# Performance work log

Hardware: AMD Instinct MI355X
Metric: run time of the kernel (lower is better)

The kernel has to match this reference:

```python
import jax, jax.numpy as jnp
import numpy as np

B, L, E, H = 1, 2048, 512, 8
D = E // H


def setup_inputs() -> dict:
    key = jax.random.key(0)
    k0, k1, k2 = jax.random.split(key, 3)
    x = jax.random.normal(k0, (B, L, E), jnp.float32)
    W_qkv = jax.random.normal(k1, (E, 3 * E), jnp.float32) / np.sqrt(E).astype(np.float32)
    b_qkv = jnp.zeros((3 * E,), jnp.float32)
    W_out = jax.random.normal(k2, (E, E), jnp.float32) / np.sqrt(E).astype(np.float32)
    b_out = jnp.zeros((E,), jnp.float32)
    return {"x": x, "W_qkv": W_qkv, "b_qkv": b_qkv, "W_out": W_out, "b_out": b_out}


def reference(x, W_qkv, b_qkv, W_out, b_out):
    num_heads = H
    eps = 1e-6
    b, l, e = x.shape
    d = e // num_heads
    qkv = x @ W_qkv + b_qkv                      # [B, L, 3E]
    q, k, v = jnp.split(qkv, 3, axis=-1)
    q = q.reshape(b, l, num_heads, d).transpose(0, 2, 1, 3)  # [B,H,L,D]
    k = k.reshape(b, l, num_heads, d).transpose(0, 2, 1, 3)
    v = v.reshape(b, l, num_heads, d).transpose(0, 2, 1, 3)
    pos = jnp.arange(l, dtype=jnp.float32).reshape(1, 1, l, 1)
    cos_w = jnp.cos(jnp.pi / 2 * pos / l)
    sin_w = jnp.sin(jnp.pi / 2 * pos / l)
    q_prime = jax.nn.relu(q)
    k_prime = jax.nn.relu(k)

    def branch(w):
        qw = q_prime * w                          # [B,H,L,D]
        kw = k_prime * w
        kv = jnp.einsum('bhld,bhle->bhlde', kw, v)  # causal running KV state
        kv_cum = jnp.cumsum(kv, axis=2)
        ctx = jnp.einsum('bhld,bhlde->bhle', qw, kv_cum)
        nrm = jnp.einsum('bhld,bhld->bhl', qw, jnp.cumsum(kw, axis=2))
        return ctx, nrm

    ctx_cos, nrm_cos = branch(cos_w)
    ctx_sin, nrm_sin = branch(sin_w)
    out = (ctx_cos + ctx_sin) / ((nrm_cos + nrm_sin)[..., None] + eps)
    out = out.transpose(0, 2, 1, 3).reshape(b, l, e)
    return out @ W_out + b_out
```

## Files before the change

kernel.cpp:

```cpp
#include <hip/hip_runtime.h>

constexpr int L_SEQ = 2048;
constexpr int E_DIM = 512;
constexpr int H_NUM = 8;
constexpr int QKV_W = 3 * E_DIM;
constexpr int CHK = 64;
constexpr int NC = L_SEQ / CHK;
constexpr float PI_HALF = 1.5707963267948966f;

typedef __attribute__((ext_vector_type(8))) short bf16x8;
typedef __attribute__((ext_vector_type(4))) float f32x4;
typedef __attribute__((ext_vector_type(4))) short short4v;

__device__ __forceinline__ short f2bf(float f) {
  union { float f; unsigned int u; } v; v.f = f;
  unsigned int r = v.u + 0x7fffu + ((v.u >> 16) & 1u);
  return (short)(r >> 16);
}

__device__ __forceinline__ void glds16(const void* g, void* l) {
  __builtin_amdgcn_global_load_lds(
      (const __attribute__((address_space(1))) unsigned int*)g,
      (__attribute__((address_space(3))) unsigned int*)l, 16, 0, 0);
}

template <int WTM, int WTN>
__global__ __launch_bounds__(256) void gemm_mfma_bf16(
    const short* __restrict__ A, const short* __restrict__ Bt,
    const float* __restrict__ bias, float* __restrict__ C,
    int M, int N, int K) {
  constexpr int BM = WTM * 32;
  constexpr int BN = WTN * 32;
  __shared__ short As[BM * 32];
  __shared__ short Bs[BN * 32];

  const int t = threadIdx.x;
  const int wave = t >> 6;
  const int lane = t & 63;
  const int quad = lane >> 4;
  const int lr = lane & 15;

  const int row0 = blockIdx.y * BM;
  const int col0 = blockIdx.x * BN;
  const int wrow = (wave >> 1) * (BM / 2);
  const int wcol = (wave & 1) * (BN / 2);

  f32x4 acc[WTM][WTN];
#pragma unroll
  for (int m = 0; m < WTM; ++m)
#pragma unroll
    for (int n = 0; n < WTN; ++n) acc[m][n] = (f32x4){0.f, 0.f, 0.f, 0.f};

  for (int k0 = 0; k0 < K; k0 += 32) {
#pragma unroll
    for (int p = wave; p < BM / 16; p += 4) {
      const int idx = p * 64 + lane;
      const int r = idx >> 2;
      const int kq = (idx & 3) * 8;
      glds16(A + (size_t)(row0 + r) * K + k0 + kq, As + p * 512);
    }
#pragma unroll
    for (int p = wave; p < BN / 16; p += 4) {
      const int idx = p * 64 + lane;
      const int r = idx >> 2;
      const int kq = (idx & 3) * 8;
      glds16(Bt + (size_t)(col0 + r) * K + k0 + kq, Bs + p * 512);
    }
    __syncthreads();

    bf16x8 af[WTM], bf_[WTN];
#pragma unroll
    for (int m = 0; m < WTM; ++m)
      af[m] = *(const bf16x8*)(As + (wrow + m * 16 + lr) * 32 + quad * 8);
#pragma unroll
    for (int n = 0; n < WTN; ++n)
      bf_[n] = *(const bf16x8*)(Bs + (wcol + n * 16 + lr) * 32 + quad * 8);
#pragma unroll
    for (int m = 0; m < WTM; ++m)
#pragma unroll
      for (int n = 0; n < WTN; ++n)
        acc[m][n] = __builtin_amdgcn_mfma_f32_16x16x32_bf16(af[m], bf_[n], acc[m][n], 0, 0, 0);
    __syncthreads();
  }

#pragma unroll
  for (int m = 0; m < WTM; ++m) {
#pragma unroll
    for (int n = 0; n < WTN; ++n) {
      const int col = col0 + wcol + n * 16 + lr;
      const int rowb = row0 + wrow + m * 16 + quad * 4;
      const float bb = bias[col];
#pragma unroll
      for (int r = 0; r < 4; ++r)
        C[(size_t)(rowb + r) * N + col] = acc[m][n][r] + bb;
    }
  }
}

__global__ __launch_bounds__(256) void cast_x_kernel(
    const float* __restrict__ x, short* __restrict__ xb) {
  const int i = blockIdx.x * 256 + threadIdx.x;
  const float4 v = ((const float4*)x)[i];
  short4v o;
  o.x = f2bf(v.x); o.y = f2bf(v.y); o.z = f2bf(v.z); o.w = f2bf(v.w);
  ((short4v*)xb)[i] = o;
}

__global__ __launch_bounds__(256) void transpose_cast_kernel(
    const float* __restrict__ W, short* __restrict__ Wt, int R, int Cc) {
  __shared__ float tile[32][33];
  const int c0 = blockIdx.x * 32, r0 = blockIdx.y * 32;
  const int tx = threadIdx.x & 31, ty = threadIdx.x >> 5;
  for (int i = ty; i < 32; i += 8) tile[i][tx] = W[(size_t)(r0 + i) * Cc + c0 + tx];
  __syncthreads();
  for (int i = ty; i < 32; i += 8)
    Wt[(size_t)(c0 + i) * R + r0 + tx] = f2bf(tile[tx][i]);
}

__global__ __launch_bounds__(256) void chunk_kv_kernel(
    const float* __restrict__ qkv, float* __restrict__ S, float* __restrict__ ksum) {
  const int c = blockIdx.x, h = blockIdx.y;
  __shared__ float kc[64][64];
  __shared__ float ksn[64][64];
  __shared__ float vs[64][64];
  __shared__ float cwA[64], swA[64];
  const int t = threadIdx.x;

  for (int idx = t; idx < 4096; idx += 256) {
    const int i = idx >> 6, d = idx & 63;
    const float* row = qkv + (size_t)(c * 64 + i) * QKV_W;
    kc[i][d] = fmaxf(row[E_DIM + h * 64 + d], 0.f);
    vs[i][d] = row[2 * E_DIM + h * 64 + d];
  }
  if (t < 64) {
    const int l = c * 64 + t;
    const float th = PI_HALF * (float)l / (float)L_SEQ;
    cwA[t] = cosf(th);
    swA[t] = sinf(th);
  }
  __syncthreads();
  for (int idx = t; idx < 4096; idx += 256) {
    const int i = idx >> 6, d = idx & 63;
    const float kv_ = kc[i][d];
    ksn[i][d] = kv_ * swA[i];
    kc[i][d] = kv_ * cwA[i];
  }
  __syncthreads();

  const int tx = t & 15, ty = t >> 4;
  float acc_c[4][4], acc_s[4][4];
#pragma unroll
  for (int m = 0; m < 4; ++m)
#pragma unroll
    for (int n = 0; n < 4; ++n) { acc_c[m][n] = 0.f; acc_s[m][n] = 0.f; }

  for (int i = 0; i < 64; ++i) {
    const float4 ac = *(const float4*)&kc[i][ty * 4];
    const float4 as = *(const float4*)&ksn[i][ty * 4];
    const float4 b4 = *(const float4*)&vs[i][tx * 4];
    const float avc[4] = {ac.x, ac.y, ac.z, ac.w};
    const float avs[4] = {as.x, as.y, as.z, as.w};
    const float bv[4] = {b4.x, b4.y, b4.z, b4.w};
#pragma unroll
    for (int m = 0; m < 4; ++m)
#pragma unroll
      for (int n = 0; n < 4; ++n) {
        acc_c[m][n] += avc[m] * bv[n];
        acc_s[m][n] += avs[m] * bv[n];
      }
  }

  float* Sc = S + ((size_t)(h * NC + c)) * 8192;
#pragma unroll
  for (int m = 0; m < 4; ++m) {
    const int d = ty * 4 + m;
    float4 oc, os;
    oc.x = acc_c[m][0]; oc.y = acc_c[m][1]; oc.z = acc_c[m][2]; oc.w = acc_c[m][3];
    os.x = acc_s[m][0]; os.y = acc_s[m][1]; os.z = acc_s[m][2]; os.w = acc_s[m][3];
    *(float4*)&Sc[(size_t)d * 64 + tx * 4] = oc;
    *(float4*)&Sc[(size_t)(64 + d) * 64 + tx * 4] = os;
  }

  if (t < 64) {
    float sc = 0.f, ss = 0.f;
    for (int i = 0; i < 64; ++i) { sc += kc[i][t]; ss += ksn[i][t]; }
    float* Kc = ksum + (size_t)(h * NC + c) * 128;
    Kc[t] = sc;
    Kc[64 + t] = ss;
  }
}

__global__ __launch_bounds__(256) void scan_kernel(
    const float* __restrict__ S, float* __restrict__ Sp,
    const float* __restrict__ ksum, float* __restrict__ ksumP) {
  const int h = blockIdx.y;
  const int e = blockIdx.x * 256 + threadIdx.x;
  float run = 0.f;
  for (int c = 0; c < NC; ++c) {
    const size_t off = ((size_t)(h * NC + c)) * 8192 + e;
    Sp[off] = run;
    run += S[off];
  }
  if (blockIdx.x == 0 && threadIdx.x < 128) {
    const int d = threadIdx.x;
    float r2 = 0.f;
    for (int c = 0; c < NC; ++c) {
      const size_t off = (size_t)(h * NC + c) * 128 + d;
      ksumP[off] = r2;
      r2 += ksum[off];
    }
  }
}

__global__ __launch_bounds__(256) void chunk_out_kernel(
    const float* __restrict__ qkv, const float* __restrict__ Sp,
    const float* __restrict__ ksumP, short* __restrict__ attn) {
  const int c = blockIdx.x, h = blockIdx.y;
  __shared__ float qs[64][65];
  __shared__ float ksA[64][65];
  __shared__ float vs[64][64];
  __shared__ float cwA[64], swA[64], nrmA[64];
  const int t = threadIdx.x;

  for (int idx = t; idx < 4096; idx += 256) {
    const int i = idx >> 6, d = idx & 63;
    const float* row = qkv + (size_t)(c * 64 + i) * QKV_W;
    qs[i][d] = fmaxf(row[h * 64 + d], 0.f);
    ksA[i][d] = fmaxf(row[E_DIM + h * 64 + d], 0.f);
    vs[i][d] = row[2 * E_DIM + h * 64 + d];
  }
  if (t < 64) {
    const int l = c * 64 + t;
    const float th = PI_HALF * (float)l / (float)L_SEQ;
    cwA[t] = cosf(th);
    swA[t] = sinf(th);
  }
  __syncthreads();

  const int tx = t & 15, ty = t >> 4;
  float areg[4][4];
  {
    float acc[4][4];
#pragma unroll
    for (int m = 0; m < 4; ++m)
#pragma unroll
      for (int n = 0; n < 4; ++n) acc[m][n] = 0.f;
    for (int d = 0; d < 64; ++d) {
      float av[4], bv[4];
#pragma unroll
      for (int m = 0; m < 4; ++m) av[m] = qs[ty * 4 + m][d];
#pragma unroll
      for (int n = 0; n < 4; ++n) bv[n] = ksA[tx * 4 + n][d];
#pragma unroll
      for (int m = 0; m < 4; ++m)
#pragma unroll
        for (int n = 0; n < 4; ++n) acc[m][n] += av[m] * bv[n];
    }
#pragma unroll
    for (int m = 0; m < 4; ++m)
#pragma unroll
      for (int n = 0; n < 4; ++n) {
        const int i = ty * 4 + m, j = tx * 4 + n;
        const float w = cwA[i] * cwA[j] + swA[i] * swA[j];
        areg[m][n] = (j <= i) ? acc[m][n] * w : 0.f;
      }
  }
  __syncthreads();
#pragma unroll
  for (int m = 0; m < 4; ++m)
#pragma unroll
    for (int n = 0; n < 4; ++n) ksA[ty * 4 + m][tx * 4 + n] = areg[m][n];
  __syncthreads();

  if (t < 64) {
    const int i = t;
    const float* Kp = ksumP + (size_t)(h * NC + c) * 128;
    float s1 = 0.f, s2 = 0.f;
    for (int d = 0; d < 64; ++d) {
      const float q = qs[i][d];
      s1 += q * Kp[d];
      s2 += q * Kp[64 + d];
    }
    float s = cwA[i] * s1 + swA[i] * s2;
    for (int j = 0; j <= i; ++j) s += ksA[i][j];
    nrmA[i] = s;
  }
  __syncthreads();

  const float* Sc = Sp + ((size_t)(h * NC + c)) * 8192;
  float acc1[4][4], acc2[4][4], acc3[4][4];
#pragma unroll
  for (int m = 0; m < 4; ++m)
#pragma unroll
    for (int n = 0; n < 4; ++n) { acc1[m][n] = 0.f; acc2[m][n] = 0.f; acc3[m][n] = 0.f; }

  for (int d = 0; d < 64; ++d) {
    float av[4];
#pragma unroll
    for (int m = 0; m < 4; ++m) av[m] = qs[ty * 4 + m][d];
    const float4 b1 = *(const float4*)&Sc[(size_t)d * 64 + tx * 4];
    const float4 b2 = *(const float4*)&Sc[(size_t)(64 + d) * 64 + tx * 4];
    const float bv1[4] = {b1.x, b1.y, b1.z, b1.w};
    const float bv2[4] = {b2.x, b2.y, b2.z, b2.w};
#pragma unroll
    for (int m = 0; m < 4; ++m)
#pragma unroll
      for (int n = 0; n < 4; ++n) {
        acc1[m][n] += av[m] * bv1[n];
        acc2[m][n] += av[m] * bv2[n];
      }
  }
  for (int j = 0; j < 64; ++j) {
    float av[4];
#pragma unroll
    for (int m = 0; m < 4; ++m) av[m] = ksA[ty * 4 + m][j];
    const float4 b4 = *(const float4*)&vs[j][tx * 4];
    const float bv[4] = {b4.x, b4.y, b4.z, b4.w};
#pragma unroll
    for (int m = 0; m < 4; ++m)
#pragma unroll
      for (int n = 0; n < 4; ++n) acc3[m][n] += av[m] * bv[n];
  }

#pragma unroll
  for (int m = 0; m < 4; ++m) {
    const int i = ty * 4 + m;
    const float inv = 1.0f / (nrmA[i] + 1e-6f);
    const float cw = cwA[i], sw = swA[i];
    short4v o;
    o.x = f2bf((cw * acc1[m][0] + sw * acc2[m][0] + acc3[m][0]) * inv);
    o.y = f2bf((cw * acc1[m][1] + sw * acc2[m][1] + acc3[m][1]) * inv);
    o.z = f2bf((cw * acc1[m][2] + sw * acc2[m][2] + acc3[m][2]) * inv);
    o.w = f2bf((cw * acc1[m][3] + sw * acc2[m][3] + acc3[m][3]) * inv);
    *(short4v*)&attn[(size_t)(c * 64 + i) * E_DIM + h * 64 + tx * 4] = o;
  }
}

extern "C" void kernel_launch(void* const* d_in, const int* in_sizes, int n_in,
                              void* d_out, int out_size, void* d_ws, size_t ws_size,
                              hipStream_t stream) {
  (void)in_sizes; (void)n_in; (void)out_size; (void)ws_size;
  const float* x     = (const float*)d_in[0];
  const float* W_qkv = (const float*)d_in[1];
  const float* b_qkv = (const float*)d_in[2];
  const float* W_out = (const float*)d_in[3];
  const float* b_out = (const float*)d_in[4];
  float* out = (float*)d_out;

  float* ws = (float*)d_ws;
  float* qkv    = ws;
  float* S      = qkv + 3145728;
  float* Sp     = S + 2097152;
  float* ksum   = Sp + 2097152;
  float* ksumP  = ksum + 32768;
  short* attn_b = (short*)(ksumP + 32768);
  short* xb     = attn_b + 1048576;
  short* Wqkv_t = xb + 1048576;
  short* Wout_t = Wqkv_t + 786432;

  cast_x_kernel<<<1024, 256, 0, stream>>>(x, xb);
  transpose_cast_kernel<<<dim3(48, 16), 256, 0, stream>>>(W_qkv, Wqkv_t, E_DIM, QKV_W);
  transpose_cast_kernel<<<dim3(16, 16), 256, 0, stream>>>(W_out, Wout_t, E_DIM, E_DIM);

  gemm_mfma_bf16<4, 2><<<dim3(QKV_W / 64, L_SEQ / 128), 256, 0, stream>>>(
      xb, Wqkv_t, b_qkv, qkv, L_SEQ, QKV_W, E_DIM);

  chunk_kv_kernel<<<dim3(NC, H_NUM), 256, 0, stream>>>(qkv, S, ksum);

  scan_kernel<<<dim3(32, H_NUM), 256, 0, stream>>>(S, Sp, ksum, ksumP);

  chunk_out_kernel<<<dim3(NC, H_NUM), 256, 0, stream>>>(qkv, Sp, ksumP, attn_b);

  gemm_mfma_bf16<2, 2><<<dim3(E_DIM / 64, L_SEQ / 64), 256, 0, stream>>>(
      attn_b, Wout_t, b_out, out, L_SEQ, E_DIM, E_DIM);
}
```

Baseline: 127.0 us.

## Port chunked linear-attention kernels to bf16 MFMA and store prefix state in bf16

The chunk KV-state and chunk output kernels now use bf16 MFMA 16x16x32 instructions instead of scalar FP32 FMA loops. The cos and sin branches are folded into a single 128-wide concatenated Q/K, so each chunk needs one matmul for scores and one for the inter-chunk term. The scan now writes the prefix state in bf16, halving its memory traffic, and the QKV GEMM uses a larger 128x128 tile. This lowers precision of intermediate states (bf16 K, V, scores, prefix state, fast __cosf/__sinf), which risks accuracy.

```diff
diff --git a/kernel.cpp b/kernel.cpp
--- a/kernel.cpp
+++ b/kernel.cpp
@@ -16,6 +16,11 @@
   union { float f; unsigned int u; } v; v.f = f;
   unsigned int r = v.u + 0x7fffu + ((v.u >> 16) & 1u);
   return (short)(r >> 16);
+}
+__device__ __forceinline__ float bf2f(short s) {
+  union { unsigned int u; float f; } v;
+  v.u = ((unsigned int)(unsigned short)s) << 16;
+  return v.f;
 }
 
 __device__ __forceinline__ void glds16(const void* g, void* l) {
@@ -117,93 +122,79 @@
     Wt[(size_t)(c0 + i) * R + r0 + tx] = f2bf(tile[tx][i]);
 }
 
-__global__ __launch_bounds__(256) void chunk_kv_kernel(
+__global__ __launch_bounds__(256) void chunk_kv_mfma(
     const float* __restrict__ qkv, float* __restrict__ S, float* __restrict__ ksum) {
   const int c = blockIdx.x, h = blockIdx.y;
-  __shared__ float kc[64][64];
-  __shared__ float ksn[64][64];
-  __shared__ float vs[64][64];
-  __shared__ float cwA[64], swA[64];
+  __shared__ short kT[128][72];
+  __shared__ short vT[64][72];
   const int t = threadIdx.x;
-
-  for (int idx = t; idx < 4096; idx += 256) {
-    const int i = idx >> 6, d = idx & 63;
+  const int w = t >> 6, lane = t & 63, lr = lane & 15, quad = lane >> 4;
+
+#pragma unroll
+  for (int r = 0; r < 16; ++r) {
+    const int i = w + 4 * r, d = lane;
     const float* row = qkv + (size_t)(c * 64 + i) * QKV_W;
-    kc[i][d] = fmaxf(row[E_DIM + h * 64 + d], 0.f);
-    vs[i][d] = row[2 * E_DIM + h * 64 + d];
-  }
-  if (t < 64) {
-    const int l = c * 64 + t;
-    const float th = PI_HALF * (float)l / (float)L_SEQ;
-    cwA[t] = cosf(th);
-    swA[t] = sinf(th);
-  }
-  __syncthreads();
-  for (int idx = t; idx < 4096; idx += 256) {
-    const int i = idx >> 6, d = idx & 63;
-    const float kv_ = kc[i][d];
-    ksn[i][d] = kv_ * swA[i];
-    kc[i][d] = kv_ * cwA[i];
-  }
-  __syncthreads();
-
-  const int tx = t & 15, ty = t >> 4;
-  float acc_c[4][4], acc_s[4][4];
-#pragma unroll
-  for (int m = 0; m < 4; ++m)
-#pragma unroll
-    for (int n = 0; n < 4; ++n) { acc_c[m][n] = 0.f; acc_s[m][n] = 0.f; }
-
-  for (int i = 0; i < 64; ++i) {
-    const float4 ac = *(const float4*)&kc[i][ty * 4];
-    const float4 as = *(const float4*)&ksn[i][ty * 4];
-    const float4 b4 = *(const float4*)&vs[i][tx * 4];
-    const float avc[4] = {ac.x, ac.y, ac.z, ac.w};
-    const float avs[4] = {as.x, as.y, as.z, as.w};
-    const float bv[4] = {b4.x, b4.y, b4.z, b4.w};
-#pragma unroll
-    for (int m = 0; m < 4; ++m)
-#pragma unroll
-      for (int n = 0; n < 4; ++n) {
-        acc_c[m][n] += avc[m] * bv[n];
-        acc_s[m][n] += avs[m] * bv[n];
-      }
+    const float kv_ = fmaxf(row[E_DIM + h * 64 + d], 0.f);
+    const float v_ = row[2 * E_DIM + h * 64 + d];
+    const float th = PI_HALF * (float)(c * 64 + i) / (float)L_SEQ;
+    kT[d][i] = f2bf(kv_ * __cosf(th));
+    kT[64 + d][i] = f2bf(kv_ * __sinf(th));
+    vT[d][i] = f2bf(v_);
+  }
+  __syncthreads();
+
+  f32x4 acc[8];
+#pragma unroll
+  for (int n = 0; n < 8; ++n) acc[n] = (f32x4){0.f, 0.f, 0.f, 0.f};
+#pragma unroll
+  for (int kk = 0; kk < 2; ++kk) {
+    const bf16x8 av = *(const bf16x8*)&vT[16 * w + lr][kk * 32 + quad * 8];
+#pragma unroll
+    for (int n = 0; n < 8; ++n) {
+      const bf16x8 bv = *(const bf16x8*)&kT[16 * n + lr][kk * 32 + quad * 8];
+      acc[n] = __builtin_amdgcn_mfma_f32_16x16x32_bf16(av, bv, acc[n], 0, 0, 0);
+    }
   }
 
   float* Sc = S + ((size_t)(h * NC + c)) * 8192;
 #pragma unroll
-  for (int m = 0; m < 4; ++m) {
-    const int d = ty * 4 + m;
-    float4 oc, os;
-    oc.x = acc_c[m][0]; oc.y = acc_c[m][1]; oc.z = acc_c[m][2]; oc.w = acc_c[m][3];
-    os.x = acc_s[m][0]; os.y = acc_s[m][1]; os.z = acc_s[m][2]; os.w = acc_s[m][3];
-    *(float4*)&Sc[(size_t)d * 64 + tx * 4] = oc;
-    *(float4*)&Sc[(size_t)(64 + d) * 64 + tx * 4] = os;
-  }
-
-  if (t < 64) {
-    float sc = 0.f, ss = 0.f;
-    for (int i = 0; i < 64; ++i) { sc += kc[i][t]; ss += ksn[i][t]; }
-    float* Kc = ksum + (size_t)(h * NC + c) * 128;
-    Kc[t] = sc;
-    Kc[64 + t] = ss;
+  for (int n = 0; n < 8; ++n) {
+    const int dd = 16 * n + lr;
+#pragma unroll
+    for (int r = 0; r < 4; ++r) {
+      const int e = 16 * w + quad * 4 + r;
+      Sc[(size_t)e * 128 + dd] = acc[n][r];
+    }
+  }
+
+  if (t < 128) {
+    float s = 0.f;
+#pragma unroll
+    for (int j = 0; j < 8; ++j) {
+      const bf16x8 kv8 = *(const bf16x8*)&kT[t][j * 8];
+#pragma unroll
+      for (int q = 0; q < 8; ++q) s += bf2f(kv8[q]);
+    }
+    ksum[(size_t)(h * NC + c) * 128 + t] = s;
   }
 }
 
 __global__ __launch_bounds__(256) void scan_kernel(
-    const float* __restrict__ S, float* __restrict__ Sp,
+    const float* __restrict__ S, short* __restrict__ Spb,
     const float* __restrict__ ksum, float* __restrict__ ksumP) {
   const int h = blockIdx.y;
   const int e = blockIdx.x * 256 + threadIdx.x;
   float run = 0.f;
+#pragma unroll
   for (int c = 0; c < NC; ++c) {
     const size_t off = ((size_t)(h * NC + c)) * 8192 + e;
-    Sp[off] = run;
+    Spb[off] = f2bf(run);
     run += S[off];
   }
   if (blockIdx.x == 0 && threadIdx.x < 128) {
     const int d = threadIdx.x;
     float r2 = 0.f;
+#pragma unroll
     for (int c = 0; c < NC; ++c) {
       const size_t off = (size_t)(h * NC + c) * 128 + d;
       ksumP[off] = r2;
@@ -212,127 +203,114 @@
   }
 }
 
-__global__ __launch_bounds__(256) void chunk_out_kernel(
-    const float* __restrict__ qkv, const float* __restrict__ Sp,
+__global__ __launch_bounds__(256) void chunk_out_mfma(
+    const float* __restrict__ qkv, const short* __restrict__ Spb,
     const float* __restrict__ ksumP, short* __restrict__ attn) {
   const int c = blockIdx.x, h = blockIdx.y;
-  __shared__ float qs[64][65];
-  __shared__ float ksA[64][65];
-  __shared__ float vs[64][64];
-  __shared__ float cwA[64], swA[64], nrmA[64];
+  __shared__ short Qc[64][136];
+  __shared__ short Kc[64][136];
+  __shared__ short Am[64][72];
+  __shared__ short vT[64][72];
+  __shared__ float nrmP[64][4];
+  __shared__ float nrmA[64];
   const int t = threadIdx.x;
-
-  for (int idx = t; idx < 4096; idx += 256) {
-    const int i = idx >> 6, d = idx & 63;
+  const int w = t >> 6, lane = t & 63, lr = lane & 15, quad = lane >> 4;
+
+#pragma unroll
+  for (int r = 0; r < 16; ++r) {
+    const int i = w + 4 * r, d = lane;
     const float* row = qkv + (size_t)(c * 64 + i) * QKV_W;
-    qs[i][d] = fmaxf(row[h * 64 + d], 0.f);
-    ksA[i][d] = fmaxf(row[E_DIM + h * 64 + d], 0.f);
-    vs[i][d] = row[2 * E_DIM + h * 64 + d];
-  }
-  if (t < 64) {
-    const int l = c * 64 + t;
-    const float th = PI_HALF * (float)l / (float)L_SEQ;
-    cwA[t] = cosf(th);
-    swA[t] = sinf(th);
-  }
-  __syncthreads();
-
-  const int tx = t & 15, ty = t >> 4;
-  float areg[4][4];
+    const float q_ = fmaxf(row[h * 64 + d], 0.f);
+    const float k_ = fmaxf(row[E_DIM + h * 64 + d], 0.f);
+    const float v_ = row[2 * E_DIM + h * 64 + d];
+    const float th = PI_HALF * (float)(c * 64 + i) / (float)L_SEQ;
+    const float cw = __cosf(th), sw = __sinf(th);
+    Qc[i][d] = f2bf(q_ * cw);
+    Qc[i][64 + d] = f2bf(q_ * sw);
+    Kc[i][d] = f2bf(k_ * cw);
+    Kc[i][64 + d] = f2bf(k_ * sw);
+    vT[d][i] = f2bf(v_);
+  }
+  __syncthreads();
+
+  f32x4 acc_a[4];
+#pragma unroll
+  for (int n = 0; n < 4; ++n) acc_a[n] = (f32x4){0.f, 0.f, 0.f, 0.f};
+#pragma unroll
+  for (int kk = 0; kk < 4; ++kk) {
+    const bf16x8 av = *(const bf16x8*)&Qc[16 * w + lr][kk * 32 + quad * 8];
+#pragma unroll
+    for (int n = 0; n < 4; ++n) {
+      const bf16x8 bv = *(const bf16x8*)&Kc[16 * n + lr][kk * 32 + quad * 8];
+      acc_a[n] = __builtin_amdgcn_mfma_f32_16x16x32_bf16(av, bv, acc_a[n], 0, 0, 0);
+    }
+  }
+#pragma unroll
+  for (int n = 0; n < 4; ++n) {
+#pragma unroll
+    for (int r = 0; r < 4; ++r) {
+      const int gi = 16 * w + quad * 4 + r;
+      const int gj = 16 * n + lr;
+      float val = (gj <= gi) ? acc_a[n][r] : 0.f;
+      Am[gi][gj] = f2bf(val);
+      float s = val;
+      s += __shfl_xor(s, 1, 64);
+      s += __shfl_xor(s, 2, 64);
+      s += __shfl_xor(s, 4, 64);
+      s += __shfl_xor(s, 8, 64);
+      if (lr == 0) nrmP[gi][n] = s;
+    }
+  }
+
+  const short* Spc = Spb + ((size_t)(h * NC + c)) * 8192;
+  f32x4 acc_c[4];
+#pragma unroll
+  for (int n = 0; n < 4; ++n) acc_c[n] = (f32x4){0.f, 0.f, 0.f, 0.f};
+#pragma unroll
+  for (int kk = 0; kk < 4; ++kk) {
+    const bf16x8 av = *(const bf16x8*)&Qc[16 * w + lr][kk * 32 + quad * 8];
+#pragma unroll
+    for (int n = 0; n < 4; ++n) {
+      const bf16x8 bv = *(const bf16x8*)(Spc + (size_t)(16 * n + lr) * 128 + kk * 32 + quad * 8);
+      acc_c[n] = __builtin_amdgcn_mfma_f32_16x16x32_bf16(av, bv, acc_c[n], 0, 0, 0);
+    }
+  }
+  __syncthreads();
+
+#pragma unroll
+  for (int kk = 0; kk < 2; ++kk) {
+    const bf16x8 av = *(const bf16x8*)&Am[16 * w + lr][kk * 32 + quad * 8];
+#pragma unroll
+    for (int n = 0; n < 4; ++n) {
+      const bf16x8 bv = *(const bf16x8*)&vT[16 * n + lr][kk * 32 + quad * 8];
+      acc_c[n] = __builtin_amdgcn_mfma_f32_16x16x32_bf16(av, bv, acc_c[n], 0, 0, 0);
+    }
+  }
+
   {
-    float acc[4][4];
-#pragma unroll
-    for (int m = 0; m < 4; ++m)
-#pragma unroll
-      for (int n = 0; n < 4; ++n) acc[m][n] = 0.f;
-    for (int d = 0; d < 64; ++d) {
-      float av[4], bv[4];
-#pragma unroll
-      for (int m = 0; m < 4; ++m) av[m] = qs[ty * 4 + m][d];
-#pragma unroll
-      for (int n = 0; n < 4; ++n) bv[n] = ksA[tx * 4 + n][d];
-#pragma unroll
-      for (int m = 0; m < 4; ++m)
-#pragma unroll
-        for (int n = 0; n < 4; ++n) acc[m][n] += av[m] * bv[n];
-    }
-#pragma unroll
-    for (int m = 0; m < 4; ++m)
-#pragma unroll
-      for (int n = 0; n < 4; ++n) {
-        const int i = ty * 4 + m, j = tx * 4 + n;
-        const float w = cwA[i] * cwA[j] + swA[i] * swA[j];
-        areg[m][n] = (j <= i) ? acc[m][n] * w : 0.f;
-      }
-  }
-  __syncthreads();
-#pragma unroll
-  for (int m = 0; m < 4; ++m)
-#pragma unroll
-    for (int n = 0; n < 4; ++n) ksA[ty * 4 + m][tx * 4 + n] = areg[m][n];
-  __syncthreads();
-
-  if (t < 64) {
-    const int i = t;
+    const int i = t >> 2, p = t & 3;
     const float* Kp = ksumP + (size_t)(h * NC + c) * 128;
-    float s1 = 0.f, s2 = 0.f;
-    for (int d = 0; d < 64; ++d) {
-      const float q = qs[i][d];
-      s1 += q * Kp[d];
-      s2 += q * Kp[64 + d];
-    }
-    float s = cwA[i] * s1 + swA[i] * s2;
-    for (int j = 0; j <= i; ++j) s += ksA[i][j];
-    nrmA[i] = s;
-  }
-  __syncthreads();
-
-  const float* Sc = Sp + ((size_t)(h * NC + c)) * 8192;
-  float acc1[4][4], acc2[4][4], acc3[4][4];
-#pragma unroll
-  for (int m = 0; m < 4; ++m)
-#pragma unroll
-    for (int n = 0; n < 4; ++n) { acc1[m][n] = 0.f; acc2[m][n] = 0.f; acc3[m][n] = 0.f; }
-
-  for (int d = 0; d < 64; ++d) {
-    float av[4];
-#pragma unroll
-    for (int m = 0; m < 4; ++m) av[m] = qs[ty * 4 + m][d];
-    const float4 b1 = *(const float4*)&Sc[(size_t)d * 64 + tx * 4];
-    const float4 b2 = *(const float4*)&Sc[(size_t)(64 + d) * 64 + tx * 4];
-    const float bv1[4] = {b1.x, b1.y, b1.z, b1.w};
-    const float bv2[4] = {b2.x, b2.y, b2.z, b2.w};
-#pragma unroll
-    for (int m = 0; m < 4; ++m)
-#pragma unroll
-      for (int n = 0; n < 4; ++n) {
-        acc1[m][n] += av[m] * bv1[n];
-        acc2[m][n] += av[m] * bv2[n];
-      }
-  }
-  for (int j = 0; j < 64; ++j) {
-    float av[4];
-#pragma unroll
-    for (int m = 0; m < 4; ++m) av[m] = ksA[ty * 4 + m][j];
-    const float4 b4 = *(const float4*)&vs[j][tx * 4];
-    const float bv[4] = {b4.x, b4.y, b4.z, b4.w};
-#pragma unroll
-    for (int m = 0; m < 4; ++m)
-#pragma unroll
-      for (int n = 0; n < 4; ++n) acc3[m][n] += av[m] * bv[n];
-  }
-
-#pragma unroll
-  for (int m = 0; m < 4; ++m) {
-    const int i = ty * 4 + m;
-    const float inv = 1.0f / (nrmA[i] + 1e-6f);
-    const float cw = cwA[i], sw = swA[i];
-    short4v o;
-    o.x = f2bf((cw * acc1[m][0] + sw * acc2[m][0] + acc3[m][0]) * inv);
-    o.y = f2bf((cw * acc1[m][1] + sw * acc2[m][1] + acc3[m][1]) * inv);
-    o.z = f2bf((cw * acc1[m][2] + sw * acc2[m][2] + acc3[m][2]) * inv);
-    o.w = f2bf((cw * acc1[m][3] + sw * acc2[m][3] + acc3[m][3]) * inv);
-    *(short4v*)&attn[(size_t)(c * 64 + i) * E_DIM + h * 64 + tx * 4] = o;
+    float dot = 0.f;
+#pragma unroll
+    for (int jj = 0; jj < 32; ++jj) {
+      const int dd = p * 32 + jj;
+      dot += bf2f(Qc[i][dd]) * Kp[dd];
+    }
+    nrmP[i][p] += dot;
+  }
+  __syncthreads();
+  if (t < 64) nrmA[t] = nrmP[t][0] + nrmP[t][1] + nrmP[t][2] + nrmP[t][3];
+  __syncthreads();
+
+#pragma unroll
+  for (int n = 0; n < 4; ++n) {
+#pragma unroll
+    for (int r = 0; r < 4; ++r) {
+      const int gi = 16 * w + quad * 4 + r;
+      const int e = 16 * n + lr;
+      const float val = acc_c[n][r] / (nrmA[gi] + 1e-6f);
+      attn[(size_t)(c * 64 + gi) * E_DIM + h * 64 + e] = f2bf(val);
+    }
   }
 }
 
@@ -350,10 +328,10 @@
   float* ws = (float*)d_ws;
   float* qkv    = ws;
   float* S      = qkv + 3145728;
-  float* Sp     = S + 2097152;
-  float* ksum   = Sp + 2097152;
+  float* ksum   = S + 2097152;
   float* ksumP  = ksum + 32768;
-  short* attn_b = (short*)(ksumP + 32768);
+  short* Spb    = (short*)(ksumP + 32768);
+  short* attn_b = Spb + 2097152;
   short* xb     = attn_b + 1048576;
   short* Wqkv_t = xb + 1048576;
   short* Wout_t = Wqkv_t + 786432;
@@ -362,14 +340,14 @@
   transpose_cast_kernel<<<dim3(48, 16), 256, 0, stream>>>(W_qkv, Wqkv_t, E_DIM, QKV_W);
   transpose_cast_kernel<<<dim3(16, 16), 256, 0, stream>>>(W_out, Wout_t, E_DIM, E_DIM);
 
-  gemm_mfma_bf16<4, 2><<<dim3(QKV_W / 64, L_SEQ / 128), 256, 0, stream>>>(
+  gemm_mfma_bf16<4, 4><<<dim3(QKV_W / 128, L_SEQ / 128), 256, 0, stream>>>(
       xb, Wqkv_t, b_qkv, qkv, L_SEQ, QKV_W, E_DIM);
 
-  chunk_kv_kernel<<<dim3(NC, H_NUM), 256, 0, stream>>>(qkv, S, ksum);
-
-  scan_kernel<<<dim3(32, H_NUM), 256, 0, stream>>>(S, Sp, ksum, ksumP);
-
-  chunk_out_kernel<<<dim3(NC, H_NUM), 256, 0, stream>>>(qkv, Sp, ksumP, attn_b);
+  chunk_kv_mfma<<<dim3(NC, H_NUM), 256, 0, stream>>>(qkv, S, ksum);
+
+  scan_kernel<<<dim3(32, H_NUM), 256, 0, stream>>>(S, Spb, ksum, ksumP);
+
+  chunk_out_mfma<<<dim3(NC, H_NUM), 256, 0, stream>>>(qkv, Spb, ksumP, attn_b);
 
   gemm_mfma_bf16<2, 2><<<dim3(E_DIM / 64, L_SEQ / 64), 256, 0, stream>>>(
       attn_b, Wout_t, b_out, out, L_SEQ, E_DIM, E_DIM);
```

Measured after the change: 114.1 us. -10.2%, faster.
